# Performance work log

Hardware: AMD Instinct MI355X
Metric: run time of the kernel (lower is better)

## Reference

```python
import jax, jax.numpy as jnp
import numpy as np

B, CIN, COUT, H, W, K, S, P = 16, 256, 128, 64, 64, 4, 2, 1
PAD = K - 1 - P  # transposed-conv equivalent padding for the lhs-dilated conv


def setup_inputs() -> dict:
    key = jax.random.key(0)
    ks = jax.random.split(key, 13)
    return {
        "x": jax.random.normal(ks[0], (B, CIN, H, W), jnp.float32),
        "feature": jax.random.uniform(ks[1], (B, 4), jnp.float32),
        "weight": jax.random.normal(ks[2], (CIN, COUT, K, K), jnp.float32) * 0.05,
        "t_bayer": jax.random.normal(ks[3], (1, CIN, COUT, K, K), jnp.float32) * 0.05,
        "t_quad": jax.random.normal(ks[4], (1, CIN, COUT, K, K), jnp.float32) * 0.05,
        "t_nano": jax.random.normal(ks[5], (1, CIN, COUT, K, K), jnp.float32) * 0.05,
        "t_qxq": jax.random.normal(ks[6], (1, CIN, COUT, K, K), jnp.float32) * 0.05,
        "m_bayer": jax.random.uniform(ks[7], (1, CIN, COUT, 1, 1), jnp.float32),
        "m_quad": jax.random.uniform(ks[8], (1, CIN, COUT, 1, 1), jnp.float32),
        "m_nano": jax.random.uniform(ks[9], (1, CIN, COUT, 1, 1), jnp.float32),
        "m_qxq": jax.random.uniform(ks[10], (1, CIN, COUT, 1, 1), jnp.float32),
        "bias": jax.random.normal(ks[11], (COUT,), jnp.float32) * 0.05,
        "prelu_a": jnp.full((1,), 0.25, jnp.float32),
    }


def _synth_weights(feature, weight, t_bayer, t_quad, t_nano, t_qxq,
                   m_bayer, m_quad, m_nano, m_qxq):
    # feature: (B,4) softmax attention -> (B,4,1,1,1)
    sa = feature[:, :, None, None, None]
    dyn = (t_bayer * m_bayer * sa[:, 0:1]
           + t_quad * m_quad * sa[:, 1:2]
           + t_nano * m_nano * sa[:, 2:3]
           + t_qxq * m_qxq * sa[:, 3:4])  # (B, CIN, COUT, K, K)
    return weight[None] + dyn  # broadcast base weight over batch


def _deconv_per_sample(xi, wi):
    # xi: (CIN,H,W); wi: (CIN,COUT,K,K) torch conv_transpose layout.
    # conv_transpose == lhs-dilated conv with spatially-flipped, transposed kernel
    kern = jnp.flip(jnp.swapaxes(wi, 0, 1), axis=(-2, -1))  # (COUT,CIN,K,K)
    out = jax.lax.conv_general_dilated(
        xi[None], kern, window_strides=(1, 1),
        padding=[(PAD, PAD), (PAD, PAD)], lhs_dilation=(S, S),
        dimension_numbers=("NCHW", "OIHW", "NCHW"))
    return out[0]  # (COUT, H*S, W*S)


def reference(x, feature, weight, t_bayer, t_quad, t_nano, t_qxq,
              m_bayer, m_quad, m_nano, m_qxq, bias, prelu_a):
    w = _synth_weights(feature, weight, t_bayer, t_quad, t_nano, t_qxq,
                       m_bayer, m_quad, m_nano, m_qxq)
    out = jax.vmap(_deconv_per_sample)(x, w)  # (B, COUT, 128, 128)
    out = out + bias[None, :, None, None]
    # PReLU with single shared slope (torch default init 0.25)
    return jnp.where(out >= 0, out, prelu_a[0] * out)
```

## Files before the change

kernel.cpp:

```cpp
#include <hip/hip_runtime.h>
#include <hip/hip_bf16.h>
#include <cstddef>
#include <cstdint>

#define B_    16
#define CIN_  256
#define COUT_ 128
#define H_    64
#define W_    64
#define OH_   128
#define OW_   128

#define ACH   4096

typedef __attribute__((ext_vector_type(8))) short bf16x8;
typedef __attribute__((ext_vector_type(4))) float f32x4;

__device__ inline short f2bf(float f) {
    __hip_bfloat16 h = __float2bfloat16(f);
    return *reinterpret_cast<short*>(&h);
}

__device__ inline void async_ld16(const void* g, void* l) {
    typedef const __attribute__((address_space(1))) unsigned int* gp_t;
    typedef __attribute__((address_space(3))) unsigned int* lp_t;
    __builtin_amdgcn_global_load_lds((gp_t)g, (lp_t)l, 16, 0, 0);
}

__device__ inline void synth_body(
    int chunk, int cog8, int tid,
    const float* __restrict__ weight,
    const float* __restrict__ tb, const float* __restrict__ tq,
    const float* __restrict__ tn, const float* __restrict__ tx,
    const float* __restrict__ mb, const float* __restrict__ mq,
    const float* __restrict__ mn, const float* __restrict__ mx,
    const float* __restrict__ feat,
    short* __restrict__ aws,
    short* lbuf )
{
    const int ci_l = tid >> 5;
    const int co_l = (tid >> 2) & 7;
    const int kh   = tid & 3;
    const int base = (chunk*8 + ci_l) * COUT_ + cog8*8 + co_l;

    const float4 w4 = *(const float4*)(weight + (size_t)base*16 + kh*4);
    const float4 b4 = *(const float4*)(tb + (size_t)base*16 + kh*4);
    const float4 q4 = *(const float4*)(tq + (size_t)base*16 + kh*4);
    const float4 n4 = *(const float4*)(tn + (size_t)base*16 + kh*4);
    const float4 x4 = *(const float4*)(tx + (size_t)base*16 + kh*4);
    const float m_b = mb[base], m_q = mq[base];
    const float m_n = mn[base], m_x = mx[base];
    const float* wp = (const float*)&w4;
    const float* bp = (const float*)&b4;
    const float* qp = (const float*)&q4;
    const float* np = (const float*)&n4;
    const float* xp = (const float*)&x4;

    const int r  = (kh+1)&1;
    const int dh = (kh<2) ? 1 : 0;

    const int o_cls = tid >> 6;
    const int o_cor = (tid >> 3) & 7;
    const int o_e8  = tid & 7;
    const int o_off = (((cog8*8 + o_cor)*64 + o_e8*8) ^ (o_cor << 4));

    for (int b = 0; b < 16; ++b) {
        const float sb = m_b * feat[b*4+0];
        const float sq = m_q * feat[b*4+1];
        const float sn = m_n * feat[b*4+2];
        const float sx = m_x * feat[b*4+3];
        #pragma unroll
        for (int kw = 0; kw < 4; ++kw) {
            int s  = (kw+1)&1;
            int dw = (kw<2) ? 1 : 0;
            float v = wp[kw] + sb*bp[kw] + sq*qp[kw] + sn*np[kw] + sx*xp[kw];
            lbuf[((r*2+s)*8 + co_l)*32 + (dh*2+dw)*8 + ci_l] = f2bf(v);
        }
        __syncthreads();
        {
            size_t sbase = ((size_t)(b*4 + o_cls)*32 + chunk) * ACH;
            *(int2*)(aws + sbase + (o_off >> 1)) =
                *(const int2*)(lbuf + (o_cls*8 + o_cor)*32 + o_e8*4);
        }
        __syncthreads();
    }
}

__device__ inline void transform_body(
    int ihp, int b, int tid,
    const float* __restrict__ x, short* __restrict__ xt,
    float* xls )
{
    const int4 z4 = {0, 0, 0, 0};

    if (ihp == 0 || ihp == 65) {
        for (int j = tid; j < 2112; j += 256) {
            int c = j / 66, iwp = j - c*66;
            *(int4*)(xt + ((((size_t)b*32 + c)*66 + ihp)*66 + iwp)*8) = z4;
        }
        return;
    }
    if (tid < 64) {
        int c = tid >> 1, iwp = (tid & 1) * 65;
        *(int4*)(xt + ((((size_t)b*32 + c)*66 + ihp)*66 + iwp)*8) = z4;
    }
    const int ih = ihp - 1;
    for (int half = 0; half < 2; ++half) {
        __syncthreads();
        #pragma unroll
        for (int it = 0; it < 8; ++it) {
            int ci_l = it*16 + (tid >> 4);
            int iw4  = (tid & 15) * 4;
            float4 v = *(const float4*)(
                x + (((size_t)b*256 + half*128 + ci_l)*64 + ih)*64 + iw4);
            *(float4*)(xls + ci_l*68 + iw4) = v;
        }
        __syncthreads();
        #pragma unroll
        for (int it2 = 0; it2 < 4; ++it2) {
            int chunk_l = it2*4 + (tid >> 6);
            int chunk   = half*16 + chunk_l;
            int iw      = tid & 63;
            short s8[8];
            #pragma unroll
            for (int j = 0; j < 8; ++j)
                s8[j] = f2bf(xls[(chunk_l*8 + j)*68 + iw]);
            *(int4*)(xt + ((((size_t)b*32 + chunk)*66 + ihp)*66 + (iw+1))*8)
                = *(const int4*)s8;
        }
    }
}

__global__ __launch_bounds__(256) void prep_fused(
    const float* __restrict__ x,
    const float* __restrict__ weight,
    const float* __restrict__ tb, const float* __restrict__ tq,
    const float* __restrict__ tn, const float* __restrict__ tx,
    const float* __restrict__ mb, const float* __restrict__ mq,
    const float* __restrict__ mn, const float* __restrict__ mx,
    const float* __restrict__ feat,
    short* __restrict__ aws, short* __restrict__ xt)
{
    __shared__ __align__(16) char smem[34816];
    const int bid = blockIdx.x;
    const int tid = threadIdx.x;
    if (bid < 1056) {
        int ihp = bid % 66, b = bid / 66;
        transform_body(ihp, b, tid, x, xt, (float*)smem);
    } else {
        int sb = bid - 1056;
        int chunk = sb & 31, cog8 = sb >> 5;
        synth_body(chunk, cog8, tid, weight, tb, tq, tn, tx,
                   mb, mq, mn, mx, feat, aws, (short*)smem);
    }
}

__global__ __launch_bounds__(256) void synth_aws(
    const float* __restrict__ weight,
    const float* __restrict__ tb, const float* __restrict__ tq,
    const float* __restrict__ tn, const float* __restrict__ tx,
    const float* __restrict__ mb, const float* __restrict__ mq,
    const float* __restrict__ mn, const float* __restrict__ mx,
    const float* __restrict__ feat,
    short* __restrict__ aws)
{
    __shared__ __align__(16) short lbuf[4][8][32];
    synth_body(blockIdx.x, blockIdx.y, threadIdx.x, weight, tb, tq, tn, tx,
               mb, mq, mn, mx, feat, aws, &lbuf[0][0][0]);
}

__global__ __launch_bounds__(256, 2) void deconv_mfma6(
    const short* __restrict__ aws, const short* __restrict__ xt,
    const float* __restrict__ bias, const float* __restrict__ prelu_a,
    float* __restrict__ out)
{
    const int tid  = threadIdx.x;
    const int lane = tid & 63;
    const int wv   = tid >> 6;
    const int wm   = wv & 1, wn = wv >> 1;
    const int o    = blockIdx.x;
    const int x8   = o & 7;
    const int l    = o >> 3;
    const int cls  = l & 3;
    const int nt2  = (l >> 2) & 15;
    const int b    = 2*x8 + (l >> 6);
    const int a0 = (nt2 >> 1) * 8, c0 = (nt2 & 1) * 32;
    const int r = cls >> 1, s = cls & 1;

    __shared__ __align__(16) short als[2][2*ACH];
    __shared__ __align__(16) short xsb[2][2*2560];

    const short* gb[7]; size_t gstep[7]; int loff[7], isB[7], act[7];
    {
        const size_t awb = (((size_t)b*4 + cls)*32) * ACH;
        #pragma unroll
        for (int i = 0; i < 7; ++i) {
            int t = wv + i*4;
            act[i] = (t < 26);
            if (t < 16) {
                int half = t >> 3, u = t & 7;
                gb[i]    = aws + awb + half*ACH + u*512 + lane*8;
                gstep[i] = 2*ACH;  loff[i] = half*4096 + u*512;  isB[i] = 0;
            } else {
                int j = t - 16; if (j > 9) j = 9;
                int half = (j >= 5) ? 1 : 0, jj = j - half*5;
                int p = jj*64 + lane; if (p > 296) p = 296;
                int row = p / 33, col = p - row*33;
                gb[i] = xt + (((size_t)(b*32 + half)*66 + (a0 + r + row))*66
                              + (c0 + s + col)) * 8;
                gstep[i] = 2*66*66*8;  loff[i] = half*2560 + jj*512;  isB[i] = 1;
            }
        }
    }

    f32x4 acc[4][8];
    #pragma unroll
    for (int mi = 0; mi < 4; ++mi)
        #pragma unroll
        for (int ni = 0; ni < 8; ++ni)
            acc[mi][ni] = (f32x4){0.f, 0.f, 0.f, 0.f};

    const int nlo = lane & 15;
    const int q   = lane >> 4;
    const int dh  = q >> 1, dw = q & 1;

    int aoff[4];
    #pragma unroll
    for (int mi = 0; mi < 4; ++mi) {
        int row  = wm*64 + mi*16 + nlo;
        aoff[mi] = ((row*64 + q*16) ^ ((nlo & 7) << 4)) >> 1;
    }

    #pragma unroll
    for (int i = 0; i < 7; ++i)
        if (act[i])
            async_ld16(gb[i], isB[i] ? &xsb[0][loff[i]] : &als[0][loff[i]]);

    for (int c = 0; c < 16; ++c) {
        __syncthreads();
        const int sel = c & 1;
        if (c < 15) {
            const int ps = sel ^ 1;
            #pragma unroll
            for (int i = 0; i < 7; ++i)
                if (act[i])
                    async_ld16(gb[i] + (size_t)(c+1)*gstep[i],
                               isB[i] ? &xsb[ps][loff[i]] : &als[ps][loff[i]]);
        }
        #pragma unroll
        for (int h = 0; h < 2; ++h) {
            const short* ab = &als[sel][h*4096];
            const short* xb = &xsb[sel][h*2560];
            bf16x8 af[4], bfr[8];
            #pragma unroll
            for (int mi = 0; mi < 4; ++mi)
                af[mi] = *(const bf16x8*)(ab + aoff[mi]);
            #pragma unroll
            for (int ni = 0; ni < 8; ++ni) {
                int a_local = wn*4 + (ni & 3);
                int colx    = nlo + (ni >> 2)*16 + dw;
                bfr[ni] = *(const bf16x8*)(xb + ((a_local + dh)*33 + colx)*8);
            }
            #pragma unroll
            for (int mi = 0; mi < 4; ++mi)
                #pragma unroll
                for (int ni = 0; ni < 8; ++ni)
                    acc[mi][ni] = __builtin_amdgcn_mfma_f32_16x16x32_bf16(
                        af[mi], bfr[ni], acc[mi][ni], 0, 0, 0);
        }
    }

    const float pa = prelu_a[0];
    #pragma unroll
    for (int mi = 0; mi < 4; ++mi) {
        #pragma unroll
        for (int reg = 0; reg < 4; ++reg) {
            int co = wm*64 + mi*16 + q*4 + reg;
            float bv = bias[co];
            #pragma unroll
            for (int ni = 0; ni < 8; ++ni) {
                int a_local = wn*4 + (ni & 3);
                int cg      = ni >> 2;
                int oh = 2*(a0 + a_local) + r;
                int ow = 2*(c0 + cg*16 + nlo) + s;
                float v = acc[mi][ni][reg] + bv;
                v = (v >= 0.f) ? v : pa*v;
                out[(((size_t)b*COUT_ + co)*OH_ + oh)*OW_ + ow] = v;
            }
        }
    }
}

__global__ __launch_bounds__(256, 2) void deconv_mfma_gather(
    const float* __restrict__ x,
    const short* __restrict__ aws,
    const float* __restrict__ bias,
    const float* __restrict__ prelu_a,
    float* __restrict__ out)
{
    const int tid  = threadIdx.x;
    const int lane = tid & 63;
    const int wv   = tid >> 6;
    const int wm   = wv & 1, wn = wv >> 1;
    const int nt   = blockIdx.x;
    const int cls  = blockIdx.y;
    const int b    = blockIdx.z;
    const int a0 = (nt >> 2) * 8, c0 = (nt & 3) * 16;
    const int r = cls >> 1, s = cls & 1;

    __shared__ __align__(16) short xs[1280];

    int goff[5], gstep[5], gok[5];
    #pragma unroll
    for (int i = 0; i < 5; ++i) {
        int e    = tid + i*256;
        int ci_l = e & 7;
        int rc   = e >> 3;
        int row  = rc / 17;
        int col  = rc - row*17;
        int ih   = a0 - 1 + r + row;
        int iw   = c0 - 1 + s + col;
        int ok   = (rc < 153) && ((unsigned)ih < (unsigned)H_)
                              && ((unsigned)iw < (unsigned)W_);
        goff[i]  = ok ? (((b*CIN_ + ci_l)*H_ + ih)*W_ + iw) : 0;
        gstep[i] = ok ? (8*H_*W_) : 0;
        gok[i]   = ok;
    }
    const int nlo = lane & 15;
    const int q   = lane >> 4;
    const int dh  = q >> 1, dw = q & 1;

    const size_t awb = (((size_t)b*4 + cls)*32) * ACH;
    int aoff[4];
    #pragma unroll
    for (int mi = 0; mi < 4; ++mi) {
        int row  = wm*64 + mi*16 + nlo;
        aoff[mi] = ((row*64 + q*16) ^ ((nlo & 7) << 4)) >> 1;
    }

    f32x4 acc[4][4];
    #pragma unroll
    for (int mi = 0; mi < 4; ++mi)
        #pragma unroll
        for (int ni = 0; ni < 4; ++ni)
            acc[mi][ni] = (f32x4){0.f, 0.f, 0.f, 0.f};

    for (int chunk = 0; chunk < 32; ++chunk) {
        __syncthreads();
        #pragma unroll
        for (int i = 0; i < 5; ++i) {
            float v = x[goff[i] + chunk*gstep[i]];
            v = gok[i] ? v : 0.0f;
            xs[tid + i*256] = f2bf(v);
        }
        bf16x8 af[4];
        #pragma unroll
        for (int mi = 0; mi < 4; ++mi)
            af[mi] = *(const bf16x8*)(aws + awb + (size_t)chunk*ACH + aoff[mi]);
        __syncthreads();
        bf16x8 bfr[4];
        #pragma unroll
        for (int ni = 0; ni < 4; ++ni) {
            int a_local = wn*4 + ni;
            bfr[ni] = *(const bf16x8*)(xs + ((a_local + dh)*17 + (nlo + dw))*8);
        }
        #pragma unroll
        for (int mi = 0; mi < 4; ++mi)
            #pragma unroll
            for (int ni = 0; ni < 4; ++ni)
                acc[mi][ni] = __builtin_amdgcn_mfma_f32_16x16x32_bf16(
                    af[mi], bfr[ni], acc[mi][ni], 0, 0, 0);
    }

    const float pa = prelu_a[0];
    #pragma unroll
    for (int mi = 0; mi < 4; ++mi) {
        #pragma unroll
        for (int reg = 0; reg < 4; ++reg) {
            int co = wm*64 + mi*16 + q*4 + reg;
            float bv = bias[co];
            #pragma unroll
            for (int ni = 0; ni < 4; ++ni) {
                int a_local = wn*4 + ni;
                int oh = 2*(a0 + a_local) + r;
                int ow = 2*(c0 + nlo) + s;
                float v = acc[mi][ni][reg] + bv;
                v = (v >= 0.f) ? v : pa*v;
                out[(((size_t)b*COUT_ + co)*OH_ + oh)*OW_ + ow] = v;
            }
        }
    }
}

__global__ __launch_bounds__(256) void deconv_fallback(
    const float* __restrict__ x,
    const float* __restrict__ weight,
    const float* __restrict__ tb, const float* __restrict__ tq,
    const float* __restrict__ tn, const float* __restrict__ tx,
    const float* __restrict__ mb, const float* __restrict__ mq,
    const float* __restrict__ mn, const float* __restrict__ mx,
    const float* __restrict__ feat,
    const float* __restrict__ bias, const float* __restrict__ prelu_a,
    float* __restrict__ out)
{
    const int tid    = threadIdx.x;
    const int tile   = blockIdx.x;
    const int coT    = blockIdx.y;
    const int b      = blockIdx.z;
    const int tile_h = tile >> 3, tile_w = tile & 7;
    const int a0 = tile_h * 8;
    const int c0 = tile_w * 8;
    const int co0 = coT * 64;

    const int tco = tid & 15;
    const int tpx = tid >> 4;
    const int rr  = tpx >> 2, rc = tpx & 3;

    __shared__ float xsf[4][100];
    __shared__ float wsh[4][16][64];

    float acc[4][4][4];
    #pragma unroll
    for (int i = 0; i < 4; ++i)
        #pragma unroll
        for (int j = 0; j < 4; ++j)
            #pragma unroll
            for (int c = 0; c < 4; ++c) acc[i][j][c] = 0.f;

    float f0 = feat[b*4 + 0], f1 = feat[b*4 + 1];
    float f2 = feat[b*4 + 2], f3 = feat[b*4 + 3];

    for (int chunk = 0; chunk < CIN_ / 4; ++chunk) {
        const int ci0 = chunk * 4;
        __syncthreads();
        for (int e = tid; e < 400; e += 256) {
            int ci_l = e / 100; int rem = e - ci_l * 100;
            int rI = rem / 10;  int cI = rem - rI * 10;
            int ih = a0 - 1 + rI, iw = c0 - 1 + cI;
            float v = 0.f;
            if ((unsigned)ih < (unsigned)H_ && (unsigned)iw < (unsigned)W_)
                v = x[(((size_t)b * CIN_ + ci0 + ci_l) * H_ + ih) * W_ + iw];
            xsf[ci_l][rem] = v;
        }
        #pragma unroll
        for (int k = 0; k < 4; ++k) {
            int g = tid + k * 256;
            int ci_l = g >> 8; int rrem = g & 255;
            int co_l = rrem >> 2; int tg = (rrem & 3) * 4;
            int cico = (ci0 + ci_l) * COUT_ + co0 + co_l;
            int e = cico * 16 + tg;
            float4 w  = *(const float4*)(weight + e);
            float4 vb = *(const float4*)(tb + e);
            float4 vq = *(const float4*)(tq + e);
            float4 vn = *(const float4*)(tn + e);
            float4 vx = *(const float4*)(tx + e);
            float sb = mb[cico] * f0, sq = mq[cico] * f1;
            float sn = mn[cico] * f2, sx = mx[cico] * f3;
            float4 wvv;
            wvv.x = w.x + sb*vb.x + sq*vq.x + sn*vn.x + sx*vx.x;
            wvv.y = w.y + sb*vb.y + sq*vq.y + sn*vn.y + sx*vx.y;
            wvv.z = w.z + sb*vb.z + sq*vq.z + sn*vn.z + sx*vx.z;
            wvv.w = w.w + sb*vb.w + sq*vq.w + sn*vn.w + sx*vx.w;
            wsh[ci_l][tg + 0][co_l] = wvv.x;
            wsh[ci_l][tg + 1][co_l] = wvv.y;
            wsh[ci_l][tg + 2][co_l] = wvv.z;
            wsh[ci_l][tg + 3][co_l] = wvv.w;
        }
        __syncthreads();
        #pragma unroll
        for (int ci_l = 0; ci_l < 4; ++ci_l) {
            float xpv[4][4];
            #pragma unroll
            for (int i = 0; i < 4; ++i)
                #pragma unroll
                for (int j = 0; j < 4; ++j)
                    xpv[i][j] = xsf[ci_l][(rr*2 + i) * 10 + rc*2 + j];
            #pragma unroll
            for (int kh = 0; kh < 4; ++kh) {
                const int rpar = (kh & 1) ? 0 : 1;
                const int offh = (kh == 0) ? 2 : (kh == 3) ? 0 : 1;
                #pragma unroll
                for (int kw = 0; kw < 4; ++kw) {
                    const int spar = (kw & 1) ? 0 : 1;
                    const int offw = (kw == 0) ? 2 : (kw == 3) ? 0 : 1;
                    float4 wvv = *(const float4*)&wsh[ci_l][kh*4 + kw][tco*4];
                    float wr[4] = {wvv.x, wvv.y, wvv.z, wvv.w};
                    #pragma unroll
                    for (int da = 0; da < 2; ++da)
                        #pragma unroll
                        for (int dc = 0; dc < 2; ++dc) {
                            const float xvv = xpv[da + offh][dc + offw];
                            #pragma unroll
                            for (int cc = 0; cc < 4; ++cc)
                                acc[2*da + rpar][2*dc + spar][cc] =
                                    fmaf(wr[cc], xvv, acc[2*da + rpar][2*dc + spar][cc]);
                        }
                }
            }
        }
    }
    const float pa  = prelu_a[0];
    const int oh0 = tile_h * 16 + rr * 4;
    const int ow0 = tile_w * 16 + rc * 4;
    #pragma unroll
    for (int cc = 0; cc < 4; ++cc) {
        const int co = co0 + tco * 4 + cc;
        const float bv = bias[co];
        #pragma unroll
        for (int dr = 0; dr < 4; ++dr)
            #pragma unroll
            for (int dw2 = 0; dw2 < 4; ++dw2) {
                float v = acc[dr][dw2][cc] + bv;
                v = (v >= 0.f) ? v : pa * v;
                out[(((size_t)b * COUT_ + co) * OH_ + (oh0 + dr)) * OW_ + (ow0 + dw2)] = v;
            }
    }
}

extern "C" void kernel_launch(void* const* d_in, const int* in_sizes, int n_in,
                              void* d_out, int out_size, void* d_ws, size_t ws_size,
                              hipStream_t stream) {
    (void)in_sizes; (void)n_in; (void)out_size;
    const float* x      = (const float*)d_in[0];
    const float* feat   = (const float*)d_in[1];
    const float* weight = (const float*)d_in[2];
    const float* tb     = (const float*)d_in[3];
    const float* tq     = (const float*)d_in[4];
    const float* tn     = (const float*)d_in[5];
    const float* tx     = (const float*)d_in[6];
    const float* mb     = (const float*)d_in[7];
    const float* mq     = (const float*)d_in[8];
    const float* mn     = (const float*)d_in[9];
    const float* mx     = (const float*)d_in[10];
    const float* bias   = (const float*)d_in[11];
    const float* prelu  = (const float*)d_in[12];
    float* out = (float*)d_out;

    const size_t aws_sz = (size_t)B_ * 4 * 32 * ACH * sizeof(short);
    const size_t xt_sz  = (size_t)B_ * 32 * 66 * 66 * 8 * sizeof(short);

    if (ws_size >= aws_sz + xt_sz) {
        short* aws = (short*)d_ws;
        short* xt  = (short*)((char*)d_ws + aws_sz);
        prep_fused<<<dim3(1056 + 512), 256, 0, stream>>>(
            x, weight, tb, tq, tn, tx, mb, mq, mn, mx, feat, aws, xt);
        deconv_mfma6<<<dim3(1024), 256, 0, stream>>>(
            aws, xt, bias, prelu, out);
    } else if (ws_size >= aws_sz) {
        short* aws = (short*)d_ws;
        synth_aws<<<dim3(32, 16), 256, 0, stream>>>(
            weight, tb, tq, tn, tx, mb, mq, mn, mx, feat, aws);
        deconv_mfma_gather<<<dim3(32, 4, 16), 256, 0, stream>>>(
            x, aws, bias, prelu, out);
    } else {
        deconv_fallback<<<dim3(64, 2, 16), 256, 0, stream>>>(
            x, weight, tb, tq, tn, tx, mb, mq, mn, mx, feat, bias, prelu, out);
    }
}
```

Baseline: 279.3 us.

## Fuse input bf16 transform into deconv kernel, loading fp32 x directly

```diff
diff --git a/kernel.cpp b/kernel.cpp
--- a/kernel.cpp
+++ b/kernel.cpp
@@ -19,6 +19,12 @@
 __device__ inline short f2bf(float f) {
     __hip_bfloat16 h = __float2bfloat16(f);
     return *reinterpret_cast<short*>(&h);
+}
+
+__device__ inline int packbf(float lo, float hi) {
+    unsigned a = (unsigned short)f2bf(lo);
+    unsigned b = (unsigned short)f2bf(hi);
+    return (int)(a | (b << 16));
 }
 
 __device__ inline void async_ld16(const void* g, void* l) {
@@ -86,75 +92,6 @@
     }
 }
 
-__device__ inline void transform_body(
-    int ihp, int b, int tid,
-    const float* __restrict__ x, short* __restrict__ xt,
-    float* xls )
-{
-    const int4 z4 = {0, 0, 0, 0};
-
-    if (ihp == 0 || ihp == 65) {
-        for (int j = tid; j < 2112; j += 256) {
-            int c = j / 66, iwp = j - c*66;
-            *(int4*)(xt + ((((size_t)b*32 + c)*66 + ihp)*66 + iwp)*8) = z4;
-        }
-        return;
-    }
-    if (tid < 64) {
-        int c = tid >> 1, iwp = (tid & 1) * 65;
-        *(int4*)(xt + ((((size_t)b*32 + c)*66 + ihp)*66 + iwp)*8) = z4;
-    }
-    const int ih = ihp - 1;
-    for (int half = 0; half < 2; ++half) {
-        __syncthreads();
-        #pragma unroll
-        for (int it = 0; it < 8; ++it) {
-            int ci_l = it*16 + (tid >> 4);
-            int iw4  = (tid & 15) * 4;
-            float4 v = *(const float4*)(
-                x + (((size_t)b*256 + half*128 + ci_l)*64 + ih)*64 + iw4);
-            *(float4*)(xls + ci_l*68 + iw4) = v;
-        }
-        __syncthreads();
-        #pragma unroll
-        for (int it2 = 0; it2 < 4; ++it2) {
-            int chunk_l = it2*4 + (tid >> 6);
-            int chunk   = half*16 + chunk_l;
-            int iw      = tid & 63;
-            short s8[8];
-            #pragma unroll
-            for (int j = 0; j < 8; ++j)
-                s8[j] = f2bf(xls[(chunk_l*8 + j)*68 + iw]);
-            *(int4*)(xt + ((((size_t)b*32 + chunk)*66 + ihp)*66 + (iw+1))*8)
-                = *(const int4*)s8;
-        }
-    }
-}
-
-__global__ __launch_bounds__(256) void prep_fused(
-    const float* __restrict__ x,
-    const float* __restrict__ weight,
-    const float* __restrict__ tb, const float* __restrict__ tq,
-    const float* __restrict__ tn, const float* __restrict__ tx,
-    const float* __restrict__ mb, const float* __restrict__ mq,
-    const float* __restrict__ mn, const float* __restrict__ mx,
-    const float* __restrict__ feat,
-    short* __restrict__ aws, short* __restrict__ xt)
-{
-    __shared__ __align__(16) char smem[34816];
-    const int bid = blockIdx.x;
-    const int tid = threadIdx.x;
-    if (bid < 1056) {
-        int ihp = bid % 66, b = bid / 66;
-        transform_body(ihp, b, tid, x, xt, (float*)smem);
-    } else {
-        int sb = bid - 1056;
-        int chunk = sb & 31, cog8 = sb >> 5;
-        synth_body(chunk, cog8, tid, weight, tb, tq, tn, tx,
-                   mb, mq, mn, mx, feat, aws, (short*)smem);
-    }
-}
-
 __global__ __launch_bounds__(256) void synth_aws(
     const float* __restrict__ weight,
     const float* __restrict__ tb, const float* __restrict__ tq,
@@ -169,8 +106,9 @@
                mb, mq, mn, mx, feat, aws, &lbuf[0][0][0]);
 }
 
-__global__ __launch_bounds__(256, 2) void deconv_mfma6(
-    const short* __restrict__ aws, const short* __restrict__ xt,
+__global__ __launch_bounds__(256, 2) void deconv_mfma7(
+    const float* __restrict__ x,
+    const short* __restrict__ aws,
     const float* __restrict__ bias, const float* __restrict__ prelu_a,
     float* __restrict__ out)
 {
@@ -190,28 +128,38 @@
     __shared__ __align__(16) short als[2][2*ACH];
     __shared__ __align__(16) short xsb[2][2*2560];
 
-    const short* gb[7]; size_t gstep[7]; int loff[7], isB[7], act[7];
-    {
-        const size_t awb = (((size_t)b*4 + cls)*32) * ACH;
-        #pragma unroll
-        for (int i = 0; i < 7; ++i) {
-            int t = wv + i*4;
-            act[i] = (t < 26);
-            if (t < 16) {
-                int half = t >> 3, u = t & 7;
-                gb[i]    = aws + awb + half*ACH + u*512 + lane*8;
-                gstep[i] = 2*ACH;  loff[i] = half*4096 + u*512;  isB[i] = 0;
-            } else {
-                int j = t - 16; if (j > 9) j = 9;
-                int half = (j >= 5) ? 1 : 0, jj = j - half*5;
-                int p = jj*64 + lane; if (p > 296) p = 296;
-                int row = p / 33, col = p - row*33;
-                gb[i] = xt + (((size_t)(b*32 + half)*66 + (a0 + r + row))*66
-                              + (c0 + s + col)) * 8;
-                gstep[i] = 2*66*66*8;  loff[i] = half*2560 + jj*512;  isB[i] = 1;
-            }
-        }
-    }
+    const size_t awb = (((size_t)b*4 + cls)*32) * ACH;
+    const short* ga  = aws + awb + wv*512 + lane*8;
+
+    const int col2 = tid & 15;
+    const int cip  = (tid >> 4) & 3;
+    const int rowg = wv;
+    const int row_base = (rowg < 3) ? rowg*2 : 6;
+    const int nrows    = (rowg < 3) ? 2 : 3;
+    const int iw0  = c0 + s - 1 + 2*col2;
+    const int ok0  = (iw0 >= 0);
+    const int iwc  = ok0 ? iw0 : 0;
+    const int ihb  = a0 + r - 1;
+    int rv[3];
+    #pragma unroll
+    for (int j = 0; j < 3; ++j) {
+        int ih = ihb + row_base + j;
+        rv[j] = (j < nrows) && (ih >= 0) && (ih < 64);
+    }
+    const float* xg = x + ((size_t)b*256 + 2*cip)*4096 + iwc;
+
+    const int tl  = (tid < 144);
+    const int tt  = tl ? tid : 0;
+    const int half_t = (tt >= 72) ? 1 : 0;
+    const int rem_t  = tt - 72*half_t;
+    const int row_t  = rem_t >> 3, ci_t = rem_t & 7;
+    const int iw_t   = c0 + s + 31;
+    const int ih_t   = ihb + row_t;
+    const int okt    = tl && (iw_t < 64) && (ih_t >= 0) && (ih_t < 64);
+    const int iht_c  = (ih_t < 0) ? 0 : ((ih_t > 63) ? 63 : ih_t);
+    const int iwt_c  = (iw_t > 63) ? 63 : iw_t;
+    const size_t tbase = ((size_t)b*256 + half_t*8 + ci_t)*4096 + iht_c*64 + iwt_c;
+    const int lwt = ((row_t*33 + 32)*8 + ci_t) + half_t*2560;
 
     f32x4 acc[4][8];
     #pragma unroll
@@ -232,21 +180,60 @@
     }
 
     #pragma unroll
-    for (int i = 0; i < 7; ++i)
-        if (act[i])
-            async_ld16(gb[i], isB[i] ? &xsb[0][loff[i]] : &als[0][loff[i]]);
+    for (int i = 0; i < 4; ++i)
+        async_ld16(ga + i*2048, &als[0][wv*512 + i*2048]);
+    {
+        #pragma unroll
+        for (int h = 0; h < 2; ++h)
+            #pragma unroll
+            for (int j = 0; j < 3; ++j) {
+                float a0v = 0.f, a1v = 0.f, b0v = 0.f, b1v = 0.f;
+                if (rv[j]) {
+                    const float* p = xg + (size_t)(h*8)*4096
+                                        + (ihb + row_base + j)*64;
+                    a0v = p[0];    a1v = p[1];
+                    b0v = p[4096]; b1v = p[4097];
+                }
+                if (j < nrows) {
+                    int lb = ((row_base + j)*33 + 2*col2)*8 + 2*cip + h*2560;
+                    *(int*)&xsb[0][lb]     = ok0 ? packbf(a0v, b0v) : 0;
+                    *(int*)&xsb[0][lb + 8] = ok0 ? packbf(a1v, b1v)
+                                                 : packbf(a0v, b0v);
+                }
+            }
+        if (tl) {
+            float tv = x[tbase];
+            xsb[0][lwt] = okt ? f2bf(tv) : (short)0;
+        }
+    }
 
     for (int c = 0; c < 16; ++c) {
         __syncthreads();
         const int sel = c & 1;
+        const int ps  = sel ^ 1;
+        float ha[2][3][2], hb[2][3][2];
+        float ht = 0.f;
         if (c < 15) {
-            const int ps = sel ^ 1;
-            #pragma unroll
-            for (int i = 0; i < 7; ++i)
-                if (act[i])
-                    async_ld16(gb[i] + (size_t)(c+1)*gstep[i],
-                               isB[i] ? &xsb[ps][loff[i]] : &als[ps][loff[i]]);
-        }
+            #pragma unroll
+            for (int i = 0; i < 4; ++i)
+                async_ld16(ga + (size_t)(c+1)*2*ACH + i*2048,
+                           &als[ps][wv*512 + i*2048]);
+            #pragma unroll
+            for (int h = 0; h < 2; ++h)
+                #pragma unroll
+                for (int j = 0; j < 3; ++j) {
+                    ha[h][j][0] = ha[h][j][1] = 0.f;
+                    hb[h][j][0] = hb[h][j][1] = 0.f;
+                    if (rv[j]) {
+                        const float* p = xg + ((size_t)(c+1)*16 + h*8)*4096
+                                            + (ihb + row_base + j)*64;
+                        ha[h][j][0] = p[0];    ha[h][j][1] = p[1];
+                        hb[h][j][0] = p[4096]; hb[h][j][1] = p[4097];
+                    }
+                }
+            if (tl) ht = x[tbase + (size_t)(c+1)*65536];
+        }
+
         #pragma unroll
         for (int h = 0; h < 2; ++h) {
             const short* ab = &als[sel][h*4096];
@@ -268,6 +255,20 @@
                     acc[mi][ni] = __builtin_amdgcn_mfma_f32_16x16x32_bf16(
                         af[mi], bfr[ni], acc[mi][ni], 0, 0, 0);
         }
+
+        if (c < 15) {
+            #pragma unroll
+            for (int h = 0; h < 2; ++h)
+                #pragma unroll
+                for (int j = 0; j < 3; ++j)
+                    if (j < nrows) {
+                        int lb = ((row_base + j)*33 + 2*col2)*8 + 2*cip + h*2560;
+                        *(int*)&xsb[ps][lb]     = ok0 ? packbf(ha[h][j][0], hb[h][j][0]) : 0;
+                        *(int*)&xsb[ps][lb + 8] = ok0 ? packbf(ha[h][j][1], hb[h][j][1])
+                                                      : packbf(ha[h][j][0], hb[h][j][0]);
+                    }
+            if (tl) xsb[ps][lwt] = okt ? f2bf(ht) : (short)0;
+        }
     }
 
     const float pa = prelu_a[0];
@@ -283,107 +284,6 @@
                 int cg      = ni >> 2;
                 int oh = 2*(a0 + a_local) + r;
                 int ow = 2*(c0 + cg*16 + nlo) + s;
-                float v = acc[mi][ni][reg] + bv;
-                v = (v >= 0.f) ? v : pa*v;
-                out[(((size_t)b*COUT_ + co)*OH_ + oh)*OW_ + ow] = v;
-            }
-        }
-    }
-}
-
-__global__ __launch_bounds__(256, 2) void deconv_mfma_gather(
-    const float* __restrict__ x,
-    const short* __restrict__ aws,
-    const float* __restrict__ bias,
-    const float* __restrict__ prelu_a,
-    float* __restrict__ out)
-{
-    const int tid  = threadIdx.x;
-    const int lane = tid & 63;
-    const int wv   = tid >> 6;
-    const int wm   = wv & 1, wn = wv >> 1;
-    const int nt   = blockIdx.x;
-    const int cls  = blockIdx.y;
-    const int b    = blockIdx.z;
-    const int a0 = (nt >> 2) * 8, c0 = (nt & 3) * 16;
-    const int r = cls >> 1, s = cls & 1;
-
-    __shared__ __align__(16) short xs[1280];
-
-    int goff[5], gstep[5], gok[5];
-    #pragma unroll
-    for (int i = 0; i < 5; ++i) {
-        int e    = tid + i*256;
-        int ci_l = e & 7;
-        int rc   = e >> 3;
-        int row  = rc / 17;
-        int col  = rc - row*17;
-        int ih   = a0 - 1 + r + row;
-        int iw   = c0 - 1 + s + col;
-        int ok   = (rc < 153) && ((unsigned)ih < (unsigned)H_)
-                              && ((unsigned)iw < (unsigned)W_);
-        goff[i]  = ok ? (((b*CIN_ + ci_l)*H_ + ih)*W_ + iw) : 0;
-        gstep[i] = ok ? (8*H_*W_) : 0;
-        gok[i]   = ok;
-    }
-    const int nlo = lane & 15;
-    const int q   = lane >> 4;
-    const int dh  = q >> 1, dw = q & 1;
-
-    const size_t awb = (((size_t)b*4 + cls)*32) * ACH;
-    int aoff[4];
-    #pragma unroll
-    for (int mi = 0; mi < 4; ++mi) {
-        int row  = wm*64 + mi*16 + nlo;
-        aoff[mi] = ((row*64 + q*16) ^ ((nlo & 7) << 4)) >> 1;
-    }
-
-    f32x4 acc[4][4];
-    #pragma unroll
-    for (int mi = 0; mi < 4; ++mi)
-        #pragma unroll
-        for (int ni = 0; ni < 4; ++ni)
-            acc[mi][ni] = (f32x4){0.f, 0.f, 0.f, 0.f};
-
-    for (int chunk = 0; chunk < 32; ++chunk) {
-        __syncthreads();
-        #pragma unroll
-        for (int i = 0; i < 5; ++i) {
-            float v = x[goff[i] + chunk*gstep[i]];
-            v = gok[i] ? v : 0.0f;
-            xs[tid + i*256] = f2bf(v);
-        }
-        bf16x8 af[4];
-        #pragma unroll
-        for (int mi = 0; mi < 4; ++mi)
-            af[mi] = *(const bf16x8*)(aws + awb + (size_t)chunk*ACH + aoff[mi]);
-        __syncthreads();
-        bf16x8 bfr[4];
-        #pragma unroll
-        for (int ni = 0; ni < 4; ++ni) {
-            int a_local = wn*4 + ni;
-            bfr[ni] = *(const bf16x8*)(xs + ((a_local + dh)*17 + (nlo + dw))*8);
-        }
-        #pragma unroll
-        for (int mi = 0; mi < 4; ++mi)
-            #pragma unroll
-            for (int ni = 0; ni < 4; ++ni)
-                acc[mi][ni] = __builtin_amdgcn_mfma_f32_16x16x32_bf16(
-                    af[mi], bfr[ni], acc[mi][ni], 0, 0, 0);
-    }
-
-    const float pa = prelu_a[0];
-    #pragma unroll
-    for (int mi = 0; mi < 4; ++mi) {
-        #pragma unroll
-        for (int reg = 0; reg < 4; ++reg) {
-            int co = wm*64 + mi*16 + q*4 + reg;
-            float bv = bias[co];
-            #pragma unroll
-            for (int ni = 0; ni < 4; ++ni) {
-                int a_local = wn*4 + ni;
-                int oh = 2*(a0 + a_local) + r;
-                int ow = 2*(c0 + nlo) + s;
                 float v = acc[mi][ni][reg] + bv;
                 v = (v >= 0.f) ? v : pa*v;
                 out[(((size_t)b*COUT_ + co)*OH_ + oh)*OW_ + ow] = v;
@@ -537,20 +437,12 @@
     float* out = (float*)d_out;
 
     const size_t aws_sz = (size_t)B_ * 4 * 32 * ACH * sizeof(short);
-    const size_t xt_sz  = (size_t)B_ * 32 * 66 * 66 * 8 * sizeof(short);
-
-    if (ws_size >= aws_sz + xt_sz) {
-        short* aws = (short*)d_ws;
-        short* xt  = (short*)((char*)d_ws + aws_sz);
-        prep_fused<<<dim3(1056 + 512), 256, 0, stream>>>(
-            x, weight, tb, tq, tn, tx, mb, mq, mn, mx, feat, aws, xt);
-        deconv_mfma6<<<dim3(1024), 256, 0, stream>>>(
-            aws, xt, bias, prelu, out);
-    } else if (ws_size >= aws_sz) {
+
+    if (ws_size >= aws_sz) {
         short* aws = (short*)d_ws;
         synth_aws<<<dim3(32, 16), 256, 0, stream>>>(
             weight, tb, tq, tn, tx, mb, mq, mn, mx, feat, aws);
-        deconv_mfma_gather<<<dim3(32, 4, 16), 256, 0, stream>>>(
+        deconv_mfma7<<<dim3(1024), 256, 0, stream>>>(
             x, aws, bias, prelu, out);
     } else {
         deconv_fallback<<<dim3(64, 2, 16), 256, 0, stream>>>(
```

Measured after the change: 320.8 us. 14.9% more time.
